# Optimization experiments

Measured on AMD Instinct MI355X. Metric: run time of the kernel, lower is better.

## Reference

```python
import jax, jax.numpy as jnp
import numpy as np

K_FACTOR = 8
TOP_N = 4
NUM_LAYER = 2


def setup_inputs() -> dict:
    key = jax.random.key(0)
    ks = jax.random.split(key, 5)
    num_ent, num_rel, n_edges = 50000, 500, 500000
    emb_dim = 128
    emb_s = emb_dim // K_FACTOR  # 16
    ent_embeddings = jax.random.normal(ks[0], (num_ent, emb_dim), jnp.float32)
    rel_embeddings = jax.random.normal(ks[1], (num_rel, TOP_N * emb_s), jnp.float32)
    rel_att = jax.random.normal(ks[2], (num_rel, K_FACTOR), jnp.float32)
    edge_index = jax.random.randint(ks[3], (2, n_edges), 0, num_ent)
    edge_type = jax.random.randint(ks[4], (n_edges,), 0, num_rel)
    return dict(ent_embeddings=ent_embeddings, rel_embeddings=rel_embeddings,
                rel_att=rel_att, edge_index=edge_index, edge_type=edge_type,
                num_ent=num_ent, num_rel=num_rel)


def _segment_mean(src, idx, n):
    s = jax.ops.segment_sum(src, idx, num_segments=n)
    c = jax.ops.segment_sum(jnp.ones((src.shape[0],), src.dtype), idx, num_segments=n)
    return jnp.where(c[:, None] > 0, s / jnp.maximum(c, 1.0)[:, None], 0.0)


def _conv(x, r, r_att, ei, et, num_ent, num_rel):
    emb_dim = x.shape[1]
    s = emb_dim // K_FACTOR
    # add self-loop edges with relation id num_rel (zero embedding / zero att)
    loop = jnp.arange(num_ent, dtype=ei.dtype)
    ei = jnp.concatenate([ei, jnp.stack([loop, loop])], axis=1)
    et = jnp.concatenate([et, jnp.full((num_ent,), num_rel, et.dtype)])
    r_pad = jnp.concatenate([r, jnp.zeros((1, r.shape[1]), r.dtype)], axis=0)
    ra_pad = jnp.concatenate([r_att, jnp.zeros((1, K_FACTOR), r_att.dtype)], axis=0)

    neigh_t = x[ei[1]]          # (E, D)
    neigh_h = x[ei[0]]          # (E, D)
    neigh_r = r_pad[et]         # (E, top_n*s)
    att = jax.nn.softmax(ra_pad[et], axis=1)      # (E, k)
    order = jnp.argsort(-att, axis=-1)             # descending sort indices
    top, rem = order[:, :TOP_N], order[:, TOP_N:]

    E = neigh_h.shape[0]
    tf = neigh_t.reshape(E, K_FACTOR, s)
    hf = neigh_h.reshape(E, K_FACTOR, s)
    t_top = jnp.take_along_axis(tf, top[:, :, None], axis=1)  # (E, top_n, s)
    h_top = jnp.take_along_axis(hf, top[:, :, None], axis=1)
    h_rem = jnp.take_along_axis(hf, rem[:, :, None], axis=1)

    tmp = (h_top.reshape(E, -1) + neigh_r).reshape(E, TOP_N, s)
    rows = jnp.arange(E)[:, None]
    # the fresh random ent_embed in the original is fully overwritten by the
    # two scatters (top + remaining cover all k_factor slots) -> deterministic
    ent = (jnp.zeros((E, K_FACTOR, s), x.dtype)
           .at[rows, top].set(tmp)
           .at[rows, rem].set(h_rem))

    ent_embed = _segment_mean(ent.reshape(E, emb_dim), ei[1], num_ent)
    rel_embed = _segment_mean(t_top.reshape(E, -1) - h_top.reshape(E, -1), et, num_rel + 1)
    return jax.nn.relu(ent_embed), rel_embed[:-1], r_att


def reference(ent_embeddings, rel_embeddings, rel_att, edge_index, edge_type, num_ent, num_rel):
    x, r = ent_embeddings, rel_embeddings
    for _ in range(NUM_LAYER):
        # faithful to MAE.forward: the ORIGINAL rel_att is passed to every layer
        x, r, _ = _conv(x, r, rel_att, edge_index, edge_type, num_ent, num_rel)
    return (x, r)
```

## Files before the change

kernel.cpp:

```cpp
#include <hip/hip_runtime.h>

#define KF 8
#define TN 4
#define SDIM 16
#define EMB 128
#define NS 8
#define NB 128
#define NRMAX 512
#define SCE 1024

typedef unsigned int u32;

__device__ __forceinline__ u32 pack2bf(float a, float b) {
    u32 ua = __float_as_uint(a), ub = __float_as_uint(b);
    ua = (ua + 0x7FFFu + ((ua >> 16) & 1u)) >> 16;
    ub = (ub + 0x7FFFu + ((ub >> 16) & 1u)) >> 16;
    return ua | (ub << 16);
}
__device__ __forceinline__ float lo16(u32 w) { return __uint_as_float(w << 16); }
__device__ __forceinline__ float hi16(u32 w) { return __uint_as_float(w & 0xFFFF0000u); }

__global__ __launch_bounds__(256) void k_tobf16(const float4* __restrict__ x4, u32* __restrict__ xh, int n4) {
    int i = blockIdx.x * 256 + threadIdx.x;
    if (i >= n4) return;
    float4 v = x4[i];
    ((uint2*)xh)[i] = make_uint2(pack2bf(v.x, v.y), pack2bf(v.z, v.w));
}

__global__ void k_relmap(const float* __restrict__ rel_att, int num_rel,
                         int* __restrict__ posmap, int* __restrict__ topmap) {
    int q = blockIdx.x * blockDim.x + threadIdx.x;
    if (q >= num_rel) return;
    float v[KF]; int idx[KF];
    for (int k = 0; k < KF; ++k) { v[k] = rel_att[q * KF + k]; idx[k] = k; }
    for (int i = 1; i < KF; ++i) {
        float vi = v[i]; int ii = idx[i]; int j = i - 1;
        while (j >= 0 && v[j] < vi) { v[j + 1] = v[j]; idx[j + 1] = idx[j]; --j; }
        v[j + 1] = vi; idx[j + 1] = ii;
    }
    int pos[KF];
    for (int k = 0; k < KF; ++k) pos[k] = -1;
    for (int j = 0; j < TN; ++j) { topmap[q * TN + j] = idx[j]; pos[idx[j]] = j; }
    for (int k = 0; k < KF; ++k) posmap[q * KF + k] = pos[k];
}

__global__ __launch_bounds__(64) void k_mkpr(const float* __restrict__ r, const int* __restrict__ posmap,
                                             u32* __restrict__ prh, int num_rel) {
    int q = blockIdx.x;
    if (q >= num_rel) return;
    int i = threadIdx.x;
    int k = i >> 3;
    int pos = posmap[q * KF + k];
    u32 w = 0;
    if (pos >= 0) {
        float a = r[q * 64 + pos * SDIM + ((2 * i) & 15)];
        float b = r[q * 64 + pos * SDIM + ((2 * i + 1) & 15)];
        w = pack2bf(a, b);
    }
    prh[q * 64 + i] = w;
}

__global__ __launch_bounds__(256) void k_hist(const int* __restrict__ tails, const int* __restrict__ types,
                                              int nE, int num_rel,
                                              int* __restrict__ deg, int* __restrict__ rcnt) {
    __shared__ int hist[NRMAX];
    for (int q = threadIdx.x; q < num_rel; q += 256) hist[q] = 0;
    __syncthreads();
    for (int i = blockIdx.x * 256 + threadIdx.x; i < nE; i += gridDim.x * 256) {
        atomicAdd(&deg[tails[i]], 1);
        atomicAdd(&hist[types[i]], 1);
    }
    __syncthreads();
    for (int q = threadIdx.x; q < num_rel; q += 256) {
        int h = hist[q];
        if (h) atomicAdd(&rcnt[q], h);
    }
}

__global__ void k_scan(const int* __restrict__ in, int* __restrict__ out, int* __restrict__ out2, int n) {
    __shared__ int warp_sums[16];
    int carry = 0;
    int lane = threadIdx.x & 63, wid = threadIdx.x >> 6;
    int nw = blockDim.x >> 6;
    for (int base = 0; base < n; base += blockDim.x) {
        int i = base + (int)threadIdx.x;
        int v = (i < n) ? in[i] : 0;
        int sv = v;
        for (int o = 1; o < 64; o <<= 1) { int t = __shfl_up(sv, o, 64); if (lane >= o) sv += t; }
        if (lane == 63) warp_sums[wid] = sv;
        __syncthreads();
        if (wid == 0 && lane < nw) {
            int ws = warp_sums[lane];
            for (int o = 1; o < 16; o <<= 1) { int t = __shfl_up(ws, o, 64); if (lane >= o) ws += t; }
            warp_sums[lane] = ws;
        }
        __syncthreads();
        int wofs = (wid > 0) ? warp_sums[wid - 1] : 0;
        int total = warp_sums[nw - 1];
        if (i < n) {
            int e = carry + wofs + sv - v;
            out[i] = e;
            if (out2) out2[i] = e;
        }
        carry += total;
        __syncthreads();
    }
    if (threadIdx.x == 0) out[n] = carry;
}

__global__ __launch_bounds__(256) void k_scan1(const int* __restrict__ in, int* __restrict__ out,
                                               int* __restrict__ bsum, int n) {
    __shared__ int warp_sums[4];
    int blk = blockIdx.x;
    int i0 = blk * SCE + (int)threadIdx.x * 4;
    int v[4];
#pragma unroll
    for (int j = 0; j < 4; ++j) { int i = i0 + j; v[j] = (i < n) ? in[i] : 0; }
    int tsum = v[0] + v[1] + v[2] + v[3];
    int lane = threadIdx.x & 63, wid = threadIdx.x >> 6;
    int sv = tsum;
    for (int o = 1; o < 64; o <<= 1) { int t = __shfl_up(sv, o, 64); if (lane >= o) sv += t; }
    if (lane == 63) warp_sums[wid] = sv;
    __syncthreads();
    if (threadIdx.x == 0) {
        int s = 0;
        for (int w = 0; w < 4; ++w) { int t = warp_sums[w]; warp_sums[w] = s; s += t; }
        bsum[blk] = s;
    }
    __syncthreads();
    int run = warp_sums[wid] + sv - tsum;
#pragma unroll
    for (int j = 0; j < 4; ++j) { int i = i0 + j; if (i < n) out[i] = run; run += v[j]; }
}

__global__ __launch_bounds__(256) void k_scan2(int* __restrict__ out, int* __restrict__ out2,
                                               const int* __restrict__ bofs, int n, int nblk) {
    int blk = blockIdx.x;
    int add = bofs[blk];
    int i0 = blk * SCE + (int)threadIdx.x * 4;
#pragma unroll
    for (int j = 0; j < 4; ++j) {
        int i = i0 + j;
        if (i < n) { int val = out[i] + add; out[i] = val; out2[i] = val; }
    }
    if (blk == 0 && threadIdx.x == 0) out[n] = bofs[nblk];
}

__global__ __launch_bounds__(256) void k_scatter_tail(const int* __restrict__ heads,
                                                      const int* __restrict__ tails,
                                                      const int* __restrict__ types,
                                                      int nE, int num_ent,
                                                      int* __restrict__ tail_cur,
                                                      u32* __restrict__ tail_edges) {
    int bi = blockIdx.x;
    int xcd = bi & 7;
    int w = bi >> 3;
    int nw = gridDim.x >> 3;
    int per = (num_ent + 7) >> 3;
    int lo = xcd * per, hi = min(lo + per, num_ent);
    for (int i = w * 256 + (int)threadIdx.x; i < nE; i += nw * 256) {
        int t = tails[i];
        if (t >= lo && t < hi) {
            int p = atomicAdd(&tail_cur[t], 1);
            tail_edges[p] = (u32)heads[i] | ((u32)types[i] << 16);
        }
    }
}

__global__ __launch_bounds__(256) void k_scatter_rel(const int* __restrict__ heads,
                                                     const int* __restrict__ tails,
                                                     const int* __restrict__ types,
                                                     int nE, int num_rel,
                                                     int* __restrict__ rel_cur,
                                                     u32* __restrict__ rel_edges) {
    __shared__ int hist[NRMAX];
    __shared__ int base[NRMAX];
    int bi = blockIdx.x;
    int c = (bi & 7) * (NB >> 3) + (bi >> 3);
    int chunk = (nE + NB - 1) / NB;
    int beg = c * chunk, end = min(beg + chunk, nE);
    for (int q = threadIdx.x; q < num_rel; q += 256) hist[q] = 0;
    __syncthreads();
    for (int i = beg + (int)threadIdx.x; i < end; i += 256) atomicAdd(&hist[types[i]], 1);
    __syncthreads();
    for (int q = threadIdx.x; q < num_rel; q += 256) {
        int h = hist[q];
        base[q] = h > 0 ? atomicAdd(&rel_cur[q], h) : 0;
        hist[q] = 0;
    }
    __syncthreads();
    for (int i = beg + (int)threadIdx.x; i < end; i += 256) {
        int q = types[i];
        int rank = atomicAdd(&hist[q], 1);
        rel_edges[base[q] + rank] = (u32)tails[i] | ((u32)heads[i] << 16);
    }
}

template <bool OUT_BF16>
__global__ __launch_bounds__(256) void k_ent(const u32* __restrict__ xh, const u32* __restrict__ prh,
                                             const int* __restrict__ tail_off,
                                             const u32* __restrict__ tail_edges,
                                             u32* __restrict__ xout_h, float4* __restrict__ xout_f,
                                             int num_ent) {
    int wid = threadIdx.x >> 6;
    int t = blockIdx.x * 4 + wid;
    if (t >= num_ent) return;
    int lane = threadIdx.x & 63;
    int qw = lane >> 4, c = lane & 15;
    int beg = tail_off[t], end = tail_off[t + 1];
    int deg = end - beg;
    float acc[8] = {0.f, 0.f, 0.f, 0.f, 0.f, 0.f, 0.f, 0.f};
    for (int b2 = 0; b2 < deg; b2 += 64) {
        int m = min(64, deg - b2);
        u32 ew = (lane < m) ? tail_edges[beg + b2 + lane] : 0u;
        for (int j = 0; j < m; j += 4) {
            int idx = j + qw;
            u32 w = __shfl(ew, idx, 64);
            uint4 xr = make_uint4(0, 0, 0, 0), pr = make_uint4(0, 0, 0, 0);
            if (idx < m) {
                int h = (int)(w & 0xFFFFu);
                int q = (int)(w >> 16);
                xr = *(const uint4*)(xh + ((size_t)h << 6) + (c << 2));
                pr = *(const uint4*)(prh + ((size_t)q << 6) + (c << 2));
            }
            acc[0] += lo16(xr.x) + lo16(pr.x);
            acc[1] += hi16(xr.x) + hi16(pr.x);
            acc[2] += lo16(xr.y) + lo16(pr.y);
            acc[3] += hi16(xr.y) + hi16(pr.y);
            acc[4] += lo16(xr.z) + lo16(pr.z);
            acc[5] += hi16(xr.z) + hi16(pr.z);
            acc[6] += lo16(xr.w) + lo16(pr.w);
            acc[7] += hi16(xr.w) + hi16(pr.w);
        }
    }
#pragma unroll
    for (int d = 0; d < 8; ++d) {
        acc[d] += __shfl_xor(acc[d], 16, 64);
        acc[d] += __shfl_xor(acc[d], 32, 64);
    }
    if (qw == 0) {
        uint4 sw = *(const uint4*)(xh + ((size_t)t << 6) + (c << 2));
        float s[8] = { lo16(sw.x), hi16(sw.x), lo16(sw.y), hi16(sw.y),
                       lo16(sw.z), hi16(sw.z), lo16(sw.w), hi16(sw.w) };
        float inv = 1.f / (float)(deg + 1);
        float o[8];
#pragma unroll
        for (int d = 0; d < 8; ++d) {
            float v = (acc[d] + s[d]) * inv;
            o[d] = v > 0.f ? v : 0.f;
        }
        if (OUT_BF16) {
            uint4 ow = make_uint4(pack2bf(o[0], o[1]), pack2bf(o[2], o[3]),
                                  pack2bf(o[4], o[5]), pack2bf(o[6], o[7]));
            *(uint4*)(xout_h + ((size_t)t << 6) + (c << 2)) = ow;
        } else {
            xout_f[((size_t)t << 5) + (c << 1)]     = make_float4(o[0], o[1], o[2], o[3]);
            xout_f[((size_t)t << 5) + (c << 1) + 1] = make_float4(o[4], o[5], o[6], o[7]);
        }
    }
}

__global__ __launch_bounds__(256) void k_rel(const u32* __restrict__ xh,
                                             const int* __restrict__ rel_off,
                                             const u32* __restrict__ rel_edges,
                                             float* __restrict__ rsum) {
    int q = blockIdx.x;
    int s = blockIdx.y;
    int tid = threadIdx.x;
    int wid = tid >> 6, lane = tid & 63;
    int sub = lane >> 5, c = lane & 31;
    int beg = rel_off[q], end = rel_off[q + 1];
    int stride = (int)gridDim.y * 8;
    float4 acc = make_float4(0.f, 0.f, 0.f, 0.f);
    for (int e = beg + s * 8 + wid * 2 + sub; e < end; e += stride) {
        u32 w = rel_edges[e];
        int t = (int)(w & 0xFFFFu);
        int h = (int)(w >> 16);
        uint2 ta = *(const uint2*)(xh + ((size_t)t << 6) + (c << 1));
        uint2 hb = *(const uint2*)(xh + ((size_t)h << 6) + (c << 1));
        acc.x += lo16(ta.x) - lo16(hb.x);
        acc.y += hi16(ta.x) - hi16(hb.x);
        acc.z += lo16(ta.y) - lo16(hb.y);
        acc.w += hi16(ta.y) - hi16(hb.y);
    }
    acc.x += __shfl_xor(acc.x, 32, 64);
    acc.y += __shfl_xor(acc.y, 32, 64);
    acc.z += __shfl_xor(acc.z, 32, 64);
    acc.w += __shfl_xor(acc.w, 32, 64);
    __shared__ float4 part[4][32];
    if (sub == 0) part[wid][c] = acc;
    __syncthreads();
    if (tid < EMB) {
        const float* pf = (const float*)part;
        float v = pf[0 * EMB + tid] + pf[1 * EMB + tid] + pf[2 * EMB + tid] + pf[3 * EMB + tid];
        atomicAdd(&rsum[(size_t)q * EMB + tid], v);
    }
}

__global__ __launch_bounds__(64) void k_relfin_pr(const float* __restrict__ rsum,
                                                  const int* __restrict__ rel_off,
                                                  const int* __restrict__ posmap,
                                                  u32* __restrict__ prh, int num_rel) {
    int q = blockIdx.x;
    if (q >= num_rel) return;
    int i = threadIdx.x;
    int k = i >> 3;
    int pos = posmap[q * KF + k];
    int cnt = rel_off[q + 1] - rel_off[q];
    u32 w = 0;
    if (pos >= 0 && cnt > 0) {
        float inv = 1.f / (float)cnt;
        w = pack2bf(rsum[(size_t)q * EMB + 2 * i] * inv, rsum[(size_t)q * EMB + 2 * i + 1] * inv);
    }
    prh[q * 64 + i] = w;
}

__global__ __launch_bounds__(64) void k_relfin(const float* __restrict__ rsum,
                                               const int* __restrict__ rel_off,
                                               const int* __restrict__ topmap,
                                               float* __restrict__ rout) {
    int q = blockIdx.x;
    int t = threadIdx.x;
    int cnt = rel_off[q + 1] - rel_off[q];
    int j = t >> 4, sd = t & 15;
    int k = topmap[q * TN + j];
    float v = cnt > 0 ? rsum[(size_t)q * EMB + k * SDIM + sd] / (float)cnt : 0.f;
    rout[q * (TN * SDIM) + t] = v;
}

extern "C" void kernel_launch(void* const* d_in, const int* in_sizes, int n_in,
                              void* d_out, int out_size, void* d_ws, size_t ws_size,
                              hipStream_t stream) {
    const float* x0 = (const float*)d_in[0];
    const float* r0 = (const float*)d_in[1];
    const float* rel_att = (const float*)d_in[2];
    const int* edge_index = (const int*)d_in[3];
    const int* edge_type = (const int*)d_in[4];

    const int num_ent = in_sizes[0] / EMB;
    const int num_rel = in_sizes[2] / KF;
    const int nE = in_sizes[4];

    const int* heads = edge_index;
    const int* tails = edge_index + nE;

    const int nblk = (num_ent + SCE - 1) / SCE;

    char* base = (char*)d_ws;
    size_t off = 0;
    auto carve = [&](size_t bytes) { char* p = base + off; off = (off + bytes + 255) & ~(size_t)255; return p; };
    int* deg        = (int*)carve((size_t)num_ent * 4);
    int* tail_off   = (int*)carve((size_t)(num_ent + 1) * 4);
    int* tail_cur   = (int*)carve((size_t)num_ent * 4);
    u32* tail_edges = (u32*)carve((size_t)nE * 4);
    int* rcnt       = (int*)carve((size_t)num_rel * 4);
    int* rel_off    = (int*)carve((size_t)(num_rel + 1) * 4);
    int* rel_cur    = (int*)carve((size_t)num_rel * 4);
    u32* rel_edges  = (u32*)carve((size_t)nE * 4);
    int* posmap     = (int*)carve((size_t)num_rel * KF * 4);
    int* topmap     = (int*)carve((size_t)num_rel * TN * 4);
    int* bsum       = (int*)carve((size_t)nblk * 4);
    int* bofs       = (int*)carve((size_t)(nblk + 1) * 4);
    u32* x0h        = (u32*)carve((size_t)num_ent * EMB * 2);
    u32* x1h        = (u32*)carve((size_t)num_ent * EMB * 2);
    u32* pr0        = (u32*)carve((size_t)num_rel * 64 * 4);
    u32* pr1        = (u32*)carve((size_t)num_rel * 64 * 4);
    float* rsumA    = (float*)carve((size_t)num_rel * EMB * 4);
    float* rsumB    = (float*)carve((size_t)num_rel * EMB * 4);
    (void)ws_size;

    float* x_out = (float*)d_out;
    float* r_out = (float*)d_out + (size_t)num_ent * EMB;

    hipMemsetAsync(deg, 0, (size_t)num_ent * 4, stream);
    hipMemsetAsync(rcnt, 0, (size_t)num_rel * 4, stream);
    hipMemsetAsync(rsumA, 0, (size_t)num_rel * EMB * 4, stream);
    hipMemsetAsync(rsumB, 0, (size_t)num_rel * EMB * 4, stream);

    k_relmap<<<(num_rel + 63) / 64, 64, 0, stream>>>(rel_att, num_rel, posmap, topmap);
    k_mkpr<<<num_rel, 64, 0, stream>>>(r0, posmap, pr0, num_rel);
    k_hist<<<256, 256, 0, stream>>>(tails, edge_type, nE, num_rel, deg, rcnt);
    k_scan1<<<nblk, 256, 0, stream>>>(deg, tail_off, bsum, num_ent);
    k_scan<<<1, 256, 0, stream>>>(bsum, bofs, nullptr, nblk);
    k_scan2<<<nblk, 256, 0, stream>>>(tail_off, tail_cur, bofs, num_ent, nblk);
    k_scan<<<1, 1024, 0, stream>>>(rcnt, rel_off, rel_cur, num_rel);
    k_scatter_tail<<<512, 256, 0, stream>>>(heads, tails, edge_type, nE, num_ent, tail_cur, tail_edges);
    k_scatter_rel<<<NB, 256, 0, stream>>>(heads, tails, edge_type, nE, num_rel, rel_cur, rel_edges);
    int n4 = num_ent * 32;
    k_tobf16<<<(n4 + 255) / 256, 256, 0, stream>>>((const float4*)x0, x0h, n4);

    dim3 relgrid(num_rel, NS);
    int entgrid = (num_ent + 3) / 4;

    k_ent<true><<<entgrid, 256, 0, stream>>>(x0h, pr0, tail_off, tail_edges, x1h, nullptr, num_ent);
    k_rel<<<relgrid, 256, 0, stream>>>(x0h, rel_off, rel_edges, rsumA);
    k_relfin_pr<<<num_rel, 64, 0, stream>>>(rsumA, rel_off, posmap, pr1, num_rel);

    k_ent<false><<<entgrid, 256, 0, stream>>>(x1h, pr1, tail_off, tail_edges, nullptr, (float4*)x_out, num_ent);
    k_rel<<<relgrid, 256, 0, stream>>>(x1h, rel_off, rel_edges, rsumB);
    k_relfin<<<num_rel, 64, 0, stream>>>(rsumB, rel_off, topmap, r_out);
}
```

Measured before the change: 231.1 us.

## Fuse independent kernels into combined launches to cut launch count

```diff
diff --git a/kernel.cpp b/kernel.cpp
--- a/kernel.cpp
+++ b/kernel.cpp
@@ -6,6 +6,7 @@
 #define EMB 128
 #define NS 8
 #define NB 128
+#define NT 512
 #define NRMAX 512
 #define SCE 1024
 
@@ -20,44 +21,14 @@
 __device__ __forceinline__ float lo16(u32 w) { return __uint_as_float(w << 16); }
 __device__ __forceinline__ float hi16(u32 w) { return __uint_as_float(w & 0xFFFF0000u); }
 
-__global__ __launch_bounds__(256) void k_tobf16(const float4* __restrict__ x4, u32* __restrict__ xh, int n4) {
+__global__ __launch_bounds__(256) void k_init(int* __restrict__ deg, int num_ent,
+                                              int* __restrict__ rcnt, int num_rel,
+                                              float* __restrict__ rsumA, float* __restrict__ rsumB,
+                                              int nrsum) {
     int i = blockIdx.x * 256 + threadIdx.x;
-    if (i >= n4) return;
-    float4 v = x4[i];
-    ((uint2*)xh)[i] = make_uint2(pack2bf(v.x, v.y), pack2bf(v.z, v.w));
-}
-
-__global__ void k_relmap(const float* __restrict__ rel_att, int num_rel,
-                         int* __restrict__ posmap, int* __restrict__ topmap) {
-    int q = blockIdx.x * blockDim.x + threadIdx.x;
-    if (q >= num_rel) return;
-    float v[KF]; int idx[KF];
-    for (int k = 0; k < KF; ++k) { v[k] = rel_att[q * KF + k]; idx[k] = k; }
-    for (int i = 1; i < KF; ++i) {
-        float vi = v[i]; int ii = idx[i]; int j = i - 1;
-        while (j >= 0 && v[j] < vi) { v[j + 1] = v[j]; idx[j + 1] = idx[j]; --j; }
-        v[j + 1] = vi; idx[j + 1] = ii;
-    }
-    int pos[KF];
-    for (int k = 0; k < KF; ++k) pos[k] = -1;
-    for (int j = 0; j < TN; ++j) { topmap[q * TN + j] = idx[j]; pos[idx[j]] = j; }
-    for (int k = 0; k < KF; ++k) posmap[q * KF + k] = pos[k];
-}
-
-__global__ __launch_bounds__(64) void k_mkpr(const float* __restrict__ r, const int* __restrict__ posmap,
-                                             u32* __restrict__ prh, int num_rel) {
-    int q = blockIdx.x;
-    if (q >= num_rel) return;
-    int i = threadIdx.x;
-    int k = i >> 3;
-    int pos = posmap[q * KF + k];
-    u32 w = 0;
-    if (pos >= 0) {
-        float a = r[q * 64 + pos * SDIM + ((2 * i) & 15)];
-        float b = r[q * 64 + pos * SDIM + ((2 * i + 1) & 15)];
-        w = pack2bf(a, b);
-    }
-    prh[q * 64 + i] = w;
+    if (i < num_ent) deg[i] = 0;
+    if (i < num_rel) rcnt[i] = 0;
+    if (i < nrsum) { rsumA[i] = 0.f; rsumB[i] = 0.f; }
 }
 
 __global__ __launch_bounds__(256) void k_hist(const int* __restrict__ tails, const int* __restrict__ types,
@@ -77,7 +48,7 @@
     }
 }
 
-__global__ void k_scan(const int* __restrict__ in, int* __restrict__ out, int* __restrict__ out2, int n) {
+__device__ void scan_small(const int* __restrict__ in, int* __restrict__ out, int* __restrict__ out2, int n) {
     __shared__ int warp_sums[16];
     int carry = 0;
     int lane = threadIdx.x & 63, wid = threadIdx.x >> 6;
@@ -106,6 +77,13 @@
         __syncthreads();
     }
     if (threadIdx.x == 0) out[n] = carry;
+}
+
+__global__ void k_scan_pair(const int* __restrict__ bsum, int* __restrict__ bofs, int nblk,
+                            const int* __restrict__ rcnt, int* __restrict__ rel_off,
+                            int* __restrict__ rel_cur, int num_rel) {
+    if (blockIdx.x == 0) scan_small(bsum, bofs, nullptr, nblk);
+    else                 scan_small(rcnt, rel_off, rel_cur, num_rel);
 }
 
 __global__ __launch_bounds__(256) void k_scan1(const int* __restrict__ in, int* __restrict__ out,
@@ -146,154 +124,196 @@
     if (blk == 0 && threadIdx.x == 0) out[n] = bofs[nblk];
 }
 
-__global__ __launch_bounds__(256) void k_scatter_tail(const int* __restrict__ heads,
-                                                      const int* __restrict__ tails,
-                                                      const int* __restrict__ types,
-                                                      int nE, int num_ent,
-                                                      int* __restrict__ tail_cur,
-                                                      u32* __restrict__ tail_edges) {
-    int bi = blockIdx.x;
-    int xcd = bi & 7;
-    int w = bi >> 3;
-    int nw = gridDim.x >> 3;
-    int per = (num_ent + 7) >> 3;
-    int lo = xcd * per, hi = min(lo + per, num_ent);
-    for (int i = w * 256 + (int)threadIdx.x; i < nE; i += nw * 256) {
-        int t = tails[i];
-        if (t >= lo && t < hi) {
-            int p = atomicAdd(&tail_cur[t], 1);
-            tail_edges[p] = (u32)heads[i] | ((u32)types[i] << 16);
-        }
-    }
-}
-
-__global__ __launch_bounds__(256) void k_scatter_rel(const int* __restrict__ heads,
-                                                     const int* __restrict__ tails,
-                                                     const int* __restrict__ types,
-                                                     int nE, int num_rel,
-                                                     int* __restrict__ rel_cur,
-                                                     u32* __restrict__ rel_edges) {
-    __shared__ int hist[NRMAX];
-    __shared__ int base[NRMAX];
-    int bi = blockIdx.x;
-    int c = (bi & 7) * (NB >> 3) + (bi >> 3);
-    int chunk = (nE + NB - 1) / NB;
-    int beg = c * chunk, end = min(beg + chunk, nE);
-    for (int q = threadIdx.x; q < num_rel; q += 256) hist[q] = 0;
-    __syncthreads();
-    for (int i = beg + (int)threadIdx.x; i < end; i += 256) atomicAdd(&hist[types[i]], 1);
-    __syncthreads();
-    for (int q = threadIdx.x; q < num_rel; q += 256) {
-        int h = hist[q];
-        base[q] = h > 0 ? atomicAdd(&rel_cur[q], h) : 0;
-        hist[q] = 0;
-    }
-    __syncthreads();
-    for (int i = beg + (int)threadIdx.x; i < end; i += 256) {
-        int q = types[i];
-        int rank = atomicAdd(&hist[q], 1);
-        rel_edges[base[q] + rank] = (u32)tails[i] | ((u32)heads[i] << 16);
+__global__ __launch_bounds__(256) void k_scatter_fused(
+        const int* __restrict__ heads, const int* __restrict__ tails, const int* __restrict__ types,
+        int nE, int num_ent, int num_rel,
+        int* __restrict__ tail_cur, u32* __restrict__ tail_edges,
+        int* __restrict__ rel_cur, u32* __restrict__ rel_edges,
+        const float4* __restrict__ x4, u32* __restrict__ xh, int n4,
+        const float* __restrict__ rel_att, const float* __restrict__ r0,
+        int* __restrict__ posmap, int* __restrict__ topmap, u32* __restrict__ pr0,
+        int nc, int np) {
+    int bid = blockIdx.x;
+    if (bid < NT) {
+        int xcd = bid & 7;
+        int w = bid >> 3;
+        int nw = NT >> 3;
+        int per = (num_ent + 7) >> 3;
+        int lo = xcd * per, hi = min(lo + per, num_ent);
+        for (int i = w * 256 + (int)threadIdx.x; i < nE; i += nw * 256) {
+            int t = tails[i];
+            if (t >= lo && t < hi) {
+                int p = atomicAdd(&tail_cur[t], 1);
+                tail_edges[p] = (u32)heads[i] | ((u32)types[i] << 16);
+            }
+        }
+    } else if (bid < NT + NB) {
+        __shared__ int hist[NRMAX];
+        __shared__ int base[NRMAX];
+        int bi = bid - NT;
+        int c = (bi & 7) * (NB >> 3) + (bi >> 3);
+        int chunk = (nE + NB - 1) / NB;
+        int beg = c * chunk, end = min(beg + chunk, nE);
+        for (int q = threadIdx.x; q < num_rel; q += 256) hist[q] = 0;
+        __syncthreads();
+        for (int i = beg + (int)threadIdx.x; i < end; i += 256) atomicAdd(&hist[types[i]], 1);
+        __syncthreads();
+        for (int q = threadIdx.x; q < num_rel; q += 256) {
+            int h = hist[q];
+            base[q] = h > 0 ? atomicAdd(&rel_cur[q], h) : 0;
+            hist[q] = 0;
+        }
+        __syncthreads();
+        for (int i = beg + (int)threadIdx.x; i < end; i += 256) {
+            int q = types[i];
+            int rank = atomicAdd(&hist[q], 1);
+            rel_edges[base[q] + rank] = (u32)tails[i] | ((u32)heads[i] << 16);
+        }
+    } else if (bid < NT + NB + nc) {
+        int i = (bid - NT - NB) * 256 + (int)threadIdx.x;
+        if (i < n4) {
+            float4 v = x4[i];
+            ((uint2*)xh)[i] = make_uint2(pack2bf(v.x, v.y), pack2bf(v.z, v.w));
+        }
+    } else {
+        int q = (bid - NT - NB - nc) * 4 + ((int)threadIdx.x >> 6);
+        if (q >= num_rel) return;
+        int i = threadIdx.x & 63;
+        float v[KF]; int idx[KF];
+        for (int k = 0; k < KF; ++k) { v[k] = rel_att[q * KF + k]; idx[k] = k; }
+        for (int a = 1; a < KF; ++a) {
+            float va = v[a]; int ia = idx[a]; int j = a - 1;
+            while (j >= 0 && v[j] < va) { v[j + 1] = v[j]; idx[j + 1] = idx[j]; --j; }
+            v[j + 1] = va; idx[j + 1] = ia;
+        }
+        int pos[KF];
+        for (int k = 0; k < KF; ++k) pos[k] = -1;
+        for (int j = 0; j < TN; ++j) pos[idx[j]] = j;
+        if (i < KF) posmap[q * KF + i] = pos[i];
+        if (i < TN) topmap[q * TN + i] = idx[i];
+        int k = i >> 3;
+        int p = pos[k];
+        u32 w = 0;
+        if (p >= 0) {
+            float a = r0[q * 64 + p * SDIM + ((2 * i) & 15)];
+            float b = r0[q * 64 + p * SDIM + ((2 * i + 1) & 15)];
+            w = pack2bf(a, b);
+        }
+        pr0[q * 64 + i] = w;
     }
 }
 
 template <bool OUT_BF16>
-__global__ __launch_bounds__(256) void k_ent(const u32* __restrict__ xh, const u32* __restrict__ prh,
-                                             const int* __restrict__ tail_off,
-                                             const u32* __restrict__ tail_edges,
-                                             u32* __restrict__ xout_h, float4* __restrict__ xout_f,
-                                             int num_ent) {
-    int wid = threadIdx.x >> 6;
-    int t = blockIdx.x * 4 + wid;
-    if (t >= num_ent) return;
+__global__ __launch_bounds__(256) void k_layer(const u32* __restrict__ xh, const u32* __restrict__ prh,
+                                               const int* __restrict__ tail_off,
+                                               const u32* __restrict__ tail_edges,
+                                               const int* __restrict__ rel_off,
+                                               const u32* __restrict__ rel_edges,
+                                               float* __restrict__ rsum,
+                                               u32* __restrict__ xout_h, float4* __restrict__ xout_f,
+                                               int num_ent, int num_rel) {
+    int bid = blockIdx.x;
     int lane = threadIdx.x & 63;
     int qw = lane >> 4, c = lane & 15;
-    int beg = tail_off[t], end = tail_off[t + 1];
-    int deg = end - beg;
-    float acc[8] = {0.f, 0.f, 0.f, 0.f, 0.f, 0.f, 0.f, 0.f};
-    for (int b2 = 0; b2 < deg; b2 += 64) {
-        int m = min(64, deg - b2);
-        u32 ew = (lane < m) ? tail_edges[beg + b2 + lane] : 0u;
-        for (int j = 0; j < m; j += 4) {
-            int idx = j + qw;
-            u32 w = __shfl(ew, idx, 64);
-            uint4 xr = make_uint4(0, 0, 0, 0), pr = make_uint4(0, 0, 0, 0);
-            if (idx < m) {
-                int h = (int)(w & 0xFFFFu);
-                int q = (int)(w >> 16);
-                xr = *(const uint4*)(xh + ((size_t)h << 6) + (c << 2));
-                pr = *(const uint4*)(prh + ((size_t)q << 6) + (c << 2));
+    int wid = threadIdx.x >> 6;
+    if (bid < num_rel * NS) {
+        int q = bid >> 3, s = bid & 7;
+        int beg = rel_off[q], end = rel_off[q + 1];
+        float acc[8] = {0.f, 0.f, 0.f, 0.f, 0.f, 0.f, 0.f, 0.f};
+        int g = s * 4 + wid;
+        for (int b2 = beg + g * 64; b2 < end; b2 += 32 * 64) {
+            int m = min(64, end - b2);
+            u32 ew = (lane < m) ? rel_edges[b2 + lane] : 0u;
+            for (int j = 0; j < m; j += 4) {
+                int idx = j + qw;
+                u32 w = __shfl(ew, idx, 64);
+                uint4 ta = make_uint4(0, 0, 0, 0), hb = make_uint4(0, 0, 0, 0);
+                if (idx < m) {
+                    int t = (int)(w & 0xFFFFu);
+                    int h = (int)(w >> 16);
+                    ta = *(const uint4*)(xh + ((size_t)t << 6) + (c << 2));
+                    hb = *(const uint4*)(xh + ((size_t)h << 6) + (c << 2));
+                }
+                acc[0] += lo16(ta.x) - lo16(hb.x);
+                acc[1] += hi16(ta.x) - hi16(hb.x);
+                acc[2] += lo16(ta.y) - lo16(hb.y);
+                acc[3] += hi16(ta.y) - hi16(hb.y);
+                acc[4] += lo16(ta.z) - lo16(hb.z);
+                acc[5] += hi16(ta.z) - hi16(hb.z);
+                acc[6] += lo16(ta.w) - lo16(hb.w);
+                acc[7] += hi16(ta.w) - hi16(hb.w);
             }
-            acc[0] += lo16(xr.x) + lo16(pr.x);
-            acc[1] += hi16(xr.x) + hi16(pr.x);
-            acc[2] += lo16(xr.y) + lo16(pr.y);
-            acc[3] += hi16(xr.y) + hi16(pr.y);
-            acc[4] += lo16(xr.z) + lo16(pr.z);
-            acc[5] += hi16(xr.z) + hi16(pr.z);
-            acc[6] += lo16(xr.w) + lo16(pr.w);
-            acc[7] += hi16(xr.w) + hi16(pr.w);
-        }
-    }
-#pragma unroll
-    for (int d = 0; d < 8; ++d) {
-        acc[d] += __shfl_xor(acc[d], 16, 64);
-        acc[d] += __shfl_xor(acc[d], 32, 64);
-    }
-    if (qw == 0) {
-        uint4 sw = *(const uint4*)(xh + ((size_t)t << 6) + (c << 2));
-        float s[8] = { lo16(sw.x), hi16(sw.x), lo16(sw.y), hi16(sw.y),
-                       lo16(sw.z), hi16(sw.z), lo16(sw.w), hi16(sw.w) };
-        float inv = 1.f / (float)(deg + 1);
-        float o[8];
+        }
 #pragma unroll
         for (int d = 0; d < 8; ++d) {
-            float v = (acc[d] + s[d]) * inv;
-            o[d] = v > 0.f ? v : 0.f;
-        }
-        if (OUT_BF16) {
-            uint4 ow = make_uint4(pack2bf(o[0], o[1]), pack2bf(o[2], o[3]),
-                                  pack2bf(o[4], o[5]), pack2bf(o[6], o[7]));
-            *(uint4*)(xout_h + ((size_t)t << 6) + (c << 2)) = ow;
-        } else {
-            xout_f[((size_t)t << 5) + (c << 1)]     = make_float4(o[0], o[1], o[2], o[3]);
-            xout_f[((size_t)t << 5) + (c << 1) + 1] = make_float4(o[4], o[5], o[6], o[7]);
-        }
-    }
-}
-
-__global__ __launch_bounds__(256) void k_rel(const u32* __restrict__ xh,
-                                             const int* __restrict__ rel_off,
-                                             const u32* __restrict__ rel_edges,
-                                             float* __restrict__ rsum) {
-    int q = blockIdx.x;
-    int s = blockIdx.y;
-    int tid = threadIdx.x;
-    int wid = tid >> 6, lane = tid & 63;
-    int sub = lane >> 5, c = lane & 31;
-    int beg = rel_off[q], end = rel_off[q + 1];
-    int stride = (int)gridDim.y * 8;
-    float4 acc = make_float4(0.f, 0.f, 0.f, 0.f);
-    for (int e = beg + s * 8 + wid * 2 + sub; e < end; e += stride) {
-        u32 w = rel_edges[e];
-        int t = (int)(w & 0xFFFFu);
-        int h = (int)(w >> 16);
-        uint2 ta = *(const uint2*)(xh + ((size_t)t << 6) + (c << 1));
-        uint2 hb = *(const uint2*)(xh + ((size_t)h << 6) + (c << 1));
-        acc.x += lo16(ta.x) - lo16(hb.x);
-        acc.y += hi16(ta.x) - hi16(hb.x);
-        acc.z += lo16(ta.y) - lo16(hb.y);
-        acc.w += hi16(ta.y) - hi16(hb.y);
-    }
-    acc.x += __shfl_xor(acc.x, 32, 64);
-    acc.y += __shfl_xor(acc.y, 32, 64);
-    acc.z += __shfl_xor(acc.z, 32, 64);
-    acc.w += __shfl_xor(acc.w, 32, 64);
-    __shared__ float4 part[4][32];
-    if (sub == 0) part[wid][c] = acc;
-    __syncthreads();
-    if (tid < EMB) {
-        const float* pf = (const float*)part;
-        float v = pf[0 * EMB + tid] + pf[1 * EMB + tid] + pf[2 * EMB + tid] + pf[3 * EMB + tid];
-        atomicAdd(&rsum[(size_t)q * EMB + tid], v);
+            acc[d] += __shfl_xor(acc[d], 16, 64);
+            acc[d] += __shfl_xor(acc[d], 32, 64);
+        }
+        __shared__ float prt[4][EMB];
+        if (qw == 0) {
+#pragma unroll
+            for (int d = 0; d < 8; ++d) prt[wid][c * 8 + d] = acc[d];
+        }
+        __syncthreads();
+        int tid = threadIdx.x;
+        if (tid < EMB) {
+            float v = prt[0][tid] + prt[1][tid] + prt[2][tid] + prt[3][tid];
+            atomicAdd(&rsum[(size_t)q * EMB + tid], v);
+        }
+    } else {
+        int t = (bid - num_rel * NS) * 4 + wid;
+        if (t >= num_ent) return;
+        int beg = tail_off[t], end = tail_off[t + 1];
+        int deg = end - beg;
+        float acc[8] = {0.f, 0.f, 0.f, 0.f, 0.f, 0.f, 0.f, 0.f};
+        for (int b2 = 0; b2 < deg; b2 += 64) {
+            int m = min(64, deg - b2);
+            u32 ew = (lane < m) ? tail_edges[beg + b2 + lane] : 0u;
+            for (int j = 0; j < m; j += 4) {
+                int idx = j + qw;
+                u32 w = __shfl(ew, idx, 64);
+                uint4 xr = make_uint4(0, 0, 0, 0), pr = make_uint4(0, 0, 0, 0);
+                if (idx < m) {
+                    int h = (int)(w & 0xFFFFu);
+                    int q = (int)(w >> 16);
+                    xr = *(const uint4*)(xh + ((size_t)h << 6) + (c << 2));
+                    pr = *(const uint4*)(prh + ((size_t)q << 6) + (c << 2));
+                }
+                acc[0] += lo16(xr.x) + lo16(pr.x);
+                acc[1] += hi16(xr.x) + hi16(pr.x);
+                acc[2] += lo16(xr.y) + lo16(pr.y);
+                acc[3] += hi16(xr.y) + hi16(pr.y);
+                acc[4] += lo16(xr.z) + lo16(pr.z);
+                acc[5] += hi16(xr.z) + hi16(pr.z);
+                acc[6] += lo16(xr.w) + lo16(pr.w);
+                acc[7] += hi16(xr.w) + hi16(pr.w);
+            }
+        }
+#pragma unroll
+        for (int d = 0; d < 8; ++d) {
+            acc[d] += __shfl_xor(acc[d], 16, 64);
+            acc[d] += __shfl_xor(acc[d], 32, 64);
+        }
+        if (qw == 0) {
+            uint4 sw = *(const uint4*)(xh + ((size_t)t << 6) + (c << 2));
+            float s[8] = { lo16(sw.x), hi16(sw.x), lo16(sw.y), hi16(sw.y),
+                           lo16(sw.z), hi16(sw.z), lo16(sw.w), hi16(sw.w) };
+            float inv = 1.f / (float)(deg + 1);
+            float o[8];
+#pragma unroll
+            for (int d = 0; d < 8; ++d) {
+                float v = (acc[d] + s[d]) * inv;
+                o[d] = v > 0.f ? v : 0.f;
+            }
+            if (OUT_BF16) {
+                uint4 ow = make_uint4(pack2bf(o[0], o[1]), pack2bf(o[2], o[3]),
+                                      pack2bf(o[4], o[5]), pack2bf(o[6], o[7]));
+                *(uint4*)(xout_h + ((size_t)t << 6) + (c << 2)) = ow;
+            } else {
+                xout_f[((size_t)t << 5) + (c << 1)]     = make_float4(o[0], o[1], o[2], o[3]);
+                xout_f[((size_t)t << 5) + (c << 1) + 1] = make_float4(o[4], o[5], o[6], o[7]);
+            }
+        }
     }
 }
 
@@ -345,6 +365,9 @@
     const int* tails = edge_index + nE;
 
     const int nblk = (num_ent + SCE - 1) / SCE;
+    const int n4 = num_ent * 32;
+    const int nc = (n4 + 255) / 256;
+    const int np = (num_rel + 3) / 4;
 
     char* base = (char*)d_ws;
     size_t off = 0;
@@ -372,31 +395,25 @@
     float* x_out = (float*)d_out;
     float* r_out = (float*)d_out + (size_t)num_ent * EMB;
 
-    hipMemsetAsync(deg, 0, (size_t)num_ent * 4, stream);
-    hipMemsetAsync(rcnt, 0, (size_t)num_rel * 4, stream);
-    hipMemsetAsync(rsumA, 0, (size_t)num_rel * EMB * 4, stream);
-    hipMemsetAsync(rsumB, 0, (size_t)num_rel * EMB * 4, stream);
-
-    k_relmap<<<(num_rel + 63) / 64, 64, 0, stream>>>(rel_att, num_rel, posmap, topmap);
-    k_mkpr<<<num_rel, 64, 0, stream>>>(r0, posmap, pr0, num_rel);
+    int initmax = num_ent > num_rel * EMB ? num_ent : num_rel * EMB;
+    k_init<<<(initmax + 255) / 256, 256, 0, stream>>>(deg, num_ent, rcnt, num_rel,
+                                                      rsumA, rsumB, num_rel * EMB);
     k_hist<<<256, 256, 0, stream>>>(tails, edge_type, nE, num_rel, deg, rcnt);
     k_scan1<<<nblk, 256, 0, stream>>>(deg, tail_off, bsum, num_ent);
-    k_scan<<<1, 256, 0, stream>>>(bsum, bofs, nullptr, nblk);
+    k_scan_pair<<<2, 1024, 0, stream>>>(bsum, bofs, nblk, rcnt, rel_off, rel_cur, num_rel);
     k_scan2<<<nblk, 256, 0, stream>>>(tail_off, tail_cur, bofs, num_ent, nblk);
-    k_scan<<<1, 1024, 0, stream>>>(rcnt, rel_off, rel_cur, num_rel);
-    k_scatter_tail<<<512, 256, 0, stream>>>(heads, tails, edge_type, nE, num_ent, tail_cur, tail_edges);
-    k_scatter_rel<<<NB, 256, 0, stream>>>(heads, tails, edge_type, nE, num_rel, rel_cur, rel_edges);
-    int n4 = num_ent * 32;
-    k_tobf16<<<(n4 + 255) / 256, 256, 0, stream>>>((const float4*)x0, x0h, n4);
-
-    dim3 relgrid(num_rel, NS);
-    int entgrid = (num_ent + 3) / 4;
-
-    k_ent<true><<<entgrid, 256, 0, stream>>>(x0h, pr0, tail_off, tail_edges, x1h, nullptr, num_ent);
-    k_rel<<<relgrid, 256, 0, stream>>>(x0h, rel_off, rel_edges, rsumA);
+    k_scatter_fused<<<NT + NB + nc + np, 256, 0, stream>>>(
+        heads, tails, edge_type, nE, num_ent, num_rel,
+        tail_cur, tail_edges, rel_cur, rel_edges,
+        (const float4*)x0, x0h, n4, rel_att, r0, posmap, topmap, pr0, nc, np);
+
+    int lgrid = num_rel * NS + (num_ent + 3) / 4;
+
+    k_layer<true><<<lgrid, 256, 0, stream>>>(x0h, pr0, tail_off, tail_edges, rel_off, rel_edges,
+                                             rsumA, x1h, nullptr, num_ent, num_rel);
     k_relfin_pr<<<num_rel, 64, 0, stream>>>(rsumA, rel_off, posmap, pr1, num_rel);
 
-    k_ent<false><<<entgrid, 256, 0, stream>>>(x1h, pr1, tail_off, tail_edges, nullptr, (float4*)x_out, num_ent);
-    k_rel<<<relgrid, 256, 0, stream>>>(x1h, rel_off, rel_edges, rsumB);
+    k_layer<false><<<lgrid, 256, 0, stream>>>(x1h, pr1, tail_off, tail_edges, rel_off, rel_edges,
+                                              rsumB, nullptr, (float4*)x_out, num_ent, num_rel);
     k_relfin<<<num_rel, 64, 0, stream>>>(rsumB, rel_off, topmap, r_out);
 }
```

Result: no change. 232.2 us (+0.5%).
